# Kernel optimization log

Hardware: AMD Instinct MI355X
Metric: run time of the kernel (lower is better)

## Reference

```python
import jax, jax.numpy as jnp
import numpy as np

B, H, W, C = 8, 128, 128, 64
C3 = 3 * C            # interleaved channel count = 192
SE_R = 16             # squeeze-excite ratio


def setup_inputs() -> dict:
    key = jax.random.key(0)
    ks = jax.random.split(key, 7)
    t1 = jax.random.normal(ks[0], (B, H, W, C), dtype=jnp.float32)
    t2 = jax.random.normal(ks[1], (B, H, W, C), dtype=jnp.float32)
    t3 = jax.random.normal(ks[2], (B, H, W, C), dtype=jnp.float32)
    # SE block: two bias-free dense layers (he_normal-ish scaling)
    w_se1 = jax.random.normal(ks[3], (C3, C3 // SE_R), dtype=jnp.float32) * np.float32(np.sqrt(2.0 / C3))
    w_se2 = jax.random.normal(ks[4], (C3 // SE_R, C3), dtype=jnp.float32) * np.float32(np.sqrt(2.0 / (C3 // SE_R)))
    # Conv3D (1,1,3) stride (1,1,3) SAME on a size-1 depth dim == middle-tap
    # 1x1 conv: only kernel[...,1,:,:] multiplies real data. Keep that tap.
    w_conv = jax.random.normal(ks[5], (C3, C), dtype=jnp.float32) * np.float32(np.sqrt(1.0 / C3))
    b_conv = jnp.zeros((C,), dtype=jnp.float32)
    return {"t1": t1, "t2": t2, "t3": t3, "w_se1": w_se1, "w_se2": w_se2,
            "w_conv": w_conv, "b_conv": b_conv}


def reference(t1, t2, t3, w_se1, w_se2, w_conv, b_conv):
    b, h, w, c = t1.shape
    # Channel interleave: [t1_0, t2_0, t3_0, t1_1, t2_1, t3_1, ...]
    x = jnp.stack([t1, t2, t3], axis=-1).reshape(b, h, w, 3 * c)  # [B,H,W,3C]
    # Squeeze-excite: GAP -> dense(relu, no bias) -> dense(sigmoid, no bias) -> scale
    s = x.mean(axis=(1, 2))                       # [B,3C]
    s = jax.nn.relu(s @ w_se1)                    # [B,3C/16]
    s = jax.nn.sigmoid(s @ w_se2)                 # [B,3C]
    x = x * s[:, None, None, :]
    # Conv3D (1,1,3)/stride(1,1,3) SAME on depth-1 axis == per-pixel 3C->C matmul
    out = jax.nn.relu(jnp.einsum('bhwc,cf->bhwf', x, w_conv) + b_conv)  # [B,H,W,C]
    return out
```

## Files before the change

### kernel.cpp

```cpp
#include <hip/hip_runtime.h>
#include <hip/hip_bf16.h>

#define BQ   8
#define HW   16384
#define CIN  64
#define C3   192
#define KPB  64
#define TPB  4

typedef __attribute__((ext_vector_type(8))) short short8;
typedef __attribute__((ext_vector_type(4))) float f32x4;

__device__ __forceinline__ ushort f2bf(float f) {
    uint u = __float_as_uint(f);
    u += 0x7fffu + ((u >> 16) & 1u);
    return (ushort)(u >> 16);
}

__global__ __launch_bounds__(256) void k_reduce(const float* __restrict__ t1,
                                                const float* __restrict__ t2,
                                                const float* __restrict__ t3,
                                                float* __restrict__ partials) {
    const int bid  = blockIdx.x;
    const int b    = bid >> 6;
    const int kblk = bid & 63;
    const size_t base = (size_t)b * (size_t)(HW * CIN) + (size_t)kblk * 16384;
    const float4* s0 = (const float4*)(t1 + base);
    const float4* s1 = (const float4*)(t2 + base);
    const float4* s2 = (const float4*)(t3 + base);
    const int tid = threadIdx.x;

    float acc[3][4] = {{0.f,0.f,0.f,0.f},{0.f,0.f,0.f,0.f},{0.f,0.f,0.f,0.f}};
#pragma unroll
    for (int i = 0; i < 16; ++i) {
        const int idx = i * 256 + tid;
        float4 v0 = s0[idx];
        float4 v1 = s1[idx];
        float4 v2 = s2[idx];
        acc[0][0] += v0.x; acc[0][1] += v0.y; acc[0][2] += v0.z; acc[0][3] += v0.w;
        acc[1][0] += v1.x; acc[1][1] += v1.y; acc[1][2] += v1.z; acc[1][3] += v1.w;
        acc[2][0] += v2.x; acc[2][1] += v2.y; acc[2][2] += v2.z; acc[2][3] += v2.w;
    }
#pragma unroll
    for (int t = 0; t < 3; ++t)
#pragma unroll
        for (int j = 0; j < 4; ++j) {
            float v = acc[t][j];
            v += __shfl_xor(v, 16);
            v += __shfl_xor(v, 32);
            acc[t][j] = v;
        }

    __shared__ float red[4][C3];
    const int lane = tid & 63, wave = tid >> 6;
    if (lane < 16) {
#pragma unroll
        for (int t = 0; t < 3; ++t)
#pragma unroll
            for (int j = 0; j < 4; ++j)
                red[wave][3 * (lane * 4 + j) + t] = acc[t][j];
    }
    __syncthreads();
    if (tid < C3) {
        float v = red[0][tid] + red[1][tid] + red[2][tid] + red[3][tid];
        partials[(size_t)(b * KPB + kblk) * C3 + tid] = v;
    }
}

__global__ __launch_bounds__(256) void k_se(const float* __restrict__ partials,
                                            const float* __restrict__ w_se1,
                                            const float* __restrict__ w_se2,
                                            const float* __restrict__ w_conv,
                                            ushort* __restrict__ wbT) {
    const int b = blockIdx.x, tid = threadIdx.x;
    __shared__ float s_lds[C3];
    __shared__ float h_lds[12];
    __shared__ float sig_lds[C3];

    if (tid < C3) {
        float s = 0.f;
        const float* p = partials + (size_t)b * KPB * C3 + tid;
        for (int k = 0; k < KPB; ++k) s += p[k * C3];
        s_lds[tid] = s * (1.f / 16384.f);
    }
    __syncthreads();
    if (tid < 12) {
        float h = 0.f;
        for (int j = 0; j < C3; ++j) h += s_lds[j] * w_se1[j * 12 + tid];
        h_lds[tid] = fmaxf(h, 0.f);
    }
    __syncthreads();
    if (tid < C3) {
        float z = 0.f;
#pragma unroll
        for (int i = 0; i < 12; ++i) z += h_lds[i] * w_se2[i * C3 + tid];
        sig_lds[tid] = 1.f / (1.f + expf(-z));
    }
    __syncthreads();
    if (tid < C3) {
        const int c = tid & 63, t = tid >> 6;
        const int c3 = 3 * c + t;
        const float g = sig_lds[c3];
        ushort* dst = wbT + (size_t)b * CIN * C3;
        for (int f = 0; f < CIN; ++f)
            dst[f * C3 + tid] = f2bf(g * w_conv[c3 * CIN + f]);
    }
}

__global__ __launch_bounds__(256) void k_main(const float* __restrict__ t1,
                                              const float* __restrict__ t2,
                                              const float* __restrict__ t3,
                                              const ushort* __restrict__ wbT,
                                              const float* __restrict__ b_conv,
                                              float* __restrict__ out) {
    __shared__ ushort xs[64 * 200];
    __shared__ ushort wt[64 * 200];

    const int bid  = blockIdx.x;
    const int b    = bid >> 6;
    const int kblk = bid & 63;
    const int tid  = threadIdx.x;
    const int lane = tid & 63, wave = tid >> 6;
    const int l16  = lane & 15, lhi = lane >> 4;

    {
        const uint2* src = (const uint2*)(wbT + (size_t)b * CIN * C3);
#pragma unroll
        for (int i = 0; i < 12; ++i) {
            int ch  = i * 256 + tid;
            int row = ch / 48, col8 = ch % 48;
            *(uint2*)&wt[row * 200 + col8 * 4] = src[ch];
        }
    }

    float bias[4];
#pragma unroll
    for (int ft = 0; ft < 4; ++ft) bias[ft] = b_conv[ft * 16 + l16];

    for (int j = 0; j < TPB; ++j) {
        const int tile = kblk + j * 64;
        const size_t pbase = (size_t)b * HW + (size_t)tile * 64;
        __syncthreads();
        const float4* src0 = (const float4*)(t1 + pbase * CIN);
        const float4* src1 = (const float4*)(t2 + pbase * CIN);
        const float4* src2 = (const float4*)(t3 + pbase * CIN);
#pragma unroll
        for (int t = 0; t < 3; ++t) {
            const float4* s = (t == 0) ? src0 : (t == 1) ? src1 : src2;
#pragma unroll
            for (int i = 0; i < 4; ++i) {
                int idx = i * 256 + tid;
                float4 v = s[idx];
                int pix = idx >> 4, c = (idx & 15) * 4;
                ushort4 pk;
                pk.x = f2bf(v.x); pk.y = f2bf(v.y);
                pk.z = f2bf(v.z); pk.w = f2bf(v.w);
                *(ushort4*)&xs[pix * 200 + t * 64 + c] = pk;
            }
        }
        __syncthreads();

        f32x4 acc[4];
#pragma unroll
        for (int ft = 0; ft < 4; ++ft) acc[ft] = (f32x4){0.f, 0.f, 0.f, 0.f};
        const int arow = wave * 16 + l16;
        const int ko   = lhi * 8;
#pragma unroll
        for (int kt = 0; kt < 6; ++kt) {
            short8 a = *(const short8*)&xs[arow * 200 + kt * 32 + ko];
#pragma unroll
            for (int ft = 0; ft < 4; ++ft) {
                short8 bb = *(const short8*)&wt[(ft * 16 + l16) * 200 + kt * 32 + ko];
                acc[ft] = __builtin_amdgcn_mfma_f32_16x16x32_bf16(a, bb, acc[ft], 0, 0, 0);
            }
        }
        const size_t obase = ((size_t)b * HW + (size_t)tile * 64 + wave * 16) * CIN;
#pragma unroll
        for (int ft = 0; ft < 4; ++ft) {
#pragma unroll
            for (int r = 0; r < 4; ++r) {
                float v = acc[ft][r] + bias[ft];
                v = fmaxf(v, 0.f);
                out[obase + (size_t)(lhi * 4 + r) * CIN + ft * 16 + l16] = v;
            }
        }
    }
}

extern "C" void kernel_launch(void* const* d_in, const int* in_sizes, int n_in,
                              void* d_out, int out_size, void* d_ws, size_t ws_size,
                              hipStream_t stream) {
    (void)in_sizes; (void)n_in; (void)out_size; (void)ws_size;
    const float* t1     = (const float*)d_in[0];
    const float* t2     = (const float*)d_in[1];
    const float* t3     = (const float*)d_in[2];
    const float* w_se1  = (const float*)d_in[3];
    const float* w_se2  = (const float*)d_in[4];
    const float* w_conv = (const float*)d_in[5];
    const float* b_conv = (const float*)d_in[6];
    float* out = (float*)d_out;

    float*  partials = (float*)d_ws;
    ushort* wbT      = (ushort*)((char*)d_ws + 512 * C3 * 4);

    k_reduce<<<dim3(BQ * KPB), dim3(256), 0, stream>>>(t1, t2, t3, partials);
    k_se<<<dim3(BQ), dim3(256), 0, stream>>>(partials, w_se1, w_se2, w_conv, wbT);
    k_main<<<dim3(BQ * KPB), dim3(256), 0, stream>>>(t1, t2, t3, wbT, b_conv, out);
}
```

Before: 169.6 us.

## Fuse reduce, SE and conv into one cooperative kernel with register-held inputs

Adds a cooperative-launch kernel where each block loads its 256 pixels of all three inputs once, accumulates the channel sums, and keeps the bf16-packed data in registers. A grid-wide sync then lets every block compute the SE gates itself, build its scaled weight tile in LDS, and run the MFMA matmul from the register copy. This removes the second read of the 100MB input and the intermediate kernel launches. In exchange it holds 96 registers of data per thread, does redundant SE work in every block, and depends on all 512 blocks being co-resident, falling back to the three-kernel path otherwise.

```diff
diff --git a/kernel.cpp b/kernel.cpp
--- a/kernel.cpp
+++ b/kernel.cpp
@@ -1,12 +1,14 @@
 #include <hip/hip_runtime.h>
 #include <hip/hip_bf16.h>
+#include <hip/hip_cooperative_groups.h>
+
+namespace cg = cooperative_groups;
 
 #define BQ   8
 #define HW   16384
 #define CIN  64
 #define C3   192
 #define KPB  64
-#define TPB  4
 
 typedef __attribute__((ext_vector_type(8))) short short8;
 typedef __attribute__((ext_vector_type(4))) float f32x4;
@@ -15,6 +17,151 @@
     uint u = __float_as_uint(f);
     u += 0x7fffu + ((u >> 16) & 1u);
     return (ushort)(u >> 16);
+}
+
+__global__ __launch_bounds__(256, 2) void k_fused(
+        const float* __restrict__ t1, const float* __restrict__ t2,
+        const float* __restrict__ t3,
+        const float* __restrict__ w_se1, const float* __restrict__ w_se2,
+        const float* __restrict__ w_conv, const float* __restrict__ b_conv,
+        float* __restrict__ partials, float* __restrict__ out) {
+    __shared__ __align__(16) ushort smem[2 * 64 * 200];
+    ushort* xs = smem;
+    ushort* wt = smem + 64 * 200;
+    float* red   = (float*)smem;
+    float* smean = (float*)smem + 4 * C3;
+    float* hbuf  = (float*)smem + 5 * C3;
+    float* sigb  = (float*)smem + 5 * C3 + 12;
+
+    const int bid  = blockIdx.x;
+    const int b    = bid >> 6;
+    const int kblk = bid & 63;
+    const int tid  = threadIdx.x;
+    const int lane = tid & 63, wave = tid >> 6;
+    const int l16  = lane & 15, lhi = lane >> 4;
+
+    uint dreg[4][3][8];
+    float acc[3][4] = {{0.f,0.f,0.f,0.f},{0.f,0.f,0.f,0.f},{0.f,0.f,0.f,0.f}};
+    const size_t pixbase = (size_t)b * HW + (size_t)kblk * 256;
+#pragma unroll
+    for (int j = 0; j < 4; ++j) {
+        const size_t cb = (pixbase + (size_t)j * 64) * CIN;
+        const float4* s0 = (const float4*)(t1 + cb);
+        const float4* s1 = (const float4*)(t2 + cb);
+        const float4* s2 = (const float4*)(t3 + cb);
+#pragma unroll
+        for (int t = 0; t < 3; ++t) {
+            const float4* s = (t == 0) ? s0 : (t == 1) ? s1 : s2;
+#pragma unroll
+            for (int i = 0; i < 4; ++i) {
+                float4 v = s[i * 256 + tid];
+                acc[t][0] += v.x; acc[t][1] += v.y;
+                acc[t][2] += v.z; acc[t][3] += v.w;
+                dreg[j][t][i * 2]     = (uint)f2bf(v.x) | ((uint)f2bf(v.y) << 16);
+                dreg[j][t][i * 2 + 1] = (uint)f2bf(v.z) | ((uint)f2bf(v.w) << 16);
+            }
+        }
+    }
+#pragma unroll
+    for (int t = 0; t < 3; ++t)
+#pragma unroll
+        for (int jj = 0; jj < 4; ++jj) {
+            float v = acc[t][jj];
+            v += __shfl_xor(v, 16);
+            v += __shfl_xor(v, 32);
+            acc[t][jj] = v;
+        }
+    if (lane < 16) {
+#pragma unroll
+        for (int t = 0; t < 3; ++t)
+#pragma unroll
+            for (int jj = 0; jj < 4; ++jj)
+                red[wave * C3 + 3 * (l16 * 4 + jj) + t] = acc[t][jj];
+    }
+    __syncthreads();
+    if (tid < C3) {
+        float v = red[0 * C3 + tid] + red[1 * C3 + tid] +
+                  red[2 * C3 + tid] + red[3 * C3 + tid];
+        partials[(size_t)bid * C3 + tid] = v;
+    }
+    __threadfence();
+    cg::this_grid().sync();
+
+    if (tid < C3) {
+        const float* p = partials + (size_t)(b * KPB) * C3 + tid;
+        float s = 0.f;
+#pragma unroll 8
+        for (int k = 0; k < KPB; ++k) s += p[k * C3];
+        smean[tid] = s * (1.f / 16384.f);
+    }
+    __syncthreads();
+    if (tid < 12) {
+        float h = 0.f;
+        for (int j = 0; j < C3; ++j) h += smean[j] * w_se1[j * 12 + tid];
+        hbuf[tid] = fmaxf(h, 0.f);
+    }
+    __syncthreads();
+    if (tid < C3) {
+        float z = 0.f;
+#pragma unroll
+        for (int i = 0; i < 12; ++i) z += hbuf[i] * w_se2[i * C3 + tid];
+        sigb[tid] = 1.f / (1.f + expf(-z));
+    }
+    __syncthreads();
+    if (tid < C3) {
+        const int c = tid & 63, t = tid >> 6;
+        const int c3 = 3 * c + t;
+        const float g = sigb[c3];
+#pragma unroll
+        for (int f = 0; f < CIN; ++f)
+            wt[f * 200 + tid] = f2bf(g * w_conv[c3 * CIN + f]);
+    }
+    float bias[4];
+#pragma unroll
+    for (int ft = 0; ft < 4; ++ft) bias[ft] = b_conv[ft * 16 + l16];
+    __syncthreads();
+
+#pragma unroll
+    for (int j = 0; j < 4; ++j) {
+        if (j) __syncthreads();
+#pragma unroll
+        for (int t = 0; t < 3; ++t)
+#pragma unroll
+            for (int i = 0; i < 4; ++i) {
+                const int idx = i * 256 + tid;
+                const int pix = idx >> 4, c = (idx & 15) * 4;
+                uint2 w;
+                w.x = dreg[j][t][i * 2];
+                w.y = dreg[j][t][i * 2 + 1];
+                *(uint2*)&xs[pix * 200 + t * 64 + c] = w;
+            }
+        __syncthreads();
+
+        f32x4 a4[4];
+#pragma unroll
+        for (int ft = 0; ft < 4; ++ft) a4[ft] = (f32x4){0.f, 0.f, 0.f, 0.f};
+        const int arow = wave * 16 + l16;
+        const int ko   = lhi * 8;
+#pragma unroll
+        for (int kt = 0; kt < 6; ++kt) {
+            short8 a = *(const short8*)&xs[arow * 200 + kt * 32 + ko];
+#pragma unroll
+            for (int ft = 0; ft < 4; ++ft) {
+                short8 bb = *(const short8*)&wt[(ft * 16 + l16) * 200 + kt * 32 + ko];
+                a4[ft] = __builtin_amdgcn_mfma_f32_16x16x32_bf16(a, bb, a4[ft], 0, 0, 0);
+            }
+        }
+        const size_t obase = (pixbase + (size_t)j * 64 + wave * 16) * CIN;
+#pragma unroll
+        for (int ft = 0; ft < 4; ++ft) {
+#pragma unroll
+            for (int r = 0; r < 4; ++r) {
+                float v = a4[ft][r] + bias[ft];
+                v = fmaxf(v, 0.f);
+                out[obase + (size_t)(lhi * 4 + r) * CIN + ft * 16 + l16] = v;
+            }
+        }
+    }
 }
 
 __global__ __launch_bounds__(256) void k_reduce(const float* __restrict__ t1,
@@ -58,7 +205,7 @@
         for (int t = 0; t < 3; ++t)
 #pragma unroll
             for (int j = 0; j < 4; ++j)
-                red[wave][3 * (lane * 4 + j) + t] = acc[t][j];
+                red[wave][3 * ((lane & 15) * 4 + j) + t] = acc[t][j];
     }
     __syncthreads();
     if (tid < C3) {
@@ -137,7 +284,7 @@
 #pragma unroll
     for (int ft = 0; ft < 4; ++ft) bias[ft] = b_conv[ft * 16 + l16];
 
-    for (int j = 0; j < TPB; ++j) {
+    for (int j = 0; j < 4; ++j) {
         const int tile = kblk + j * 64;
         const size_t pbase = (size_t)b * HW + (size_t)tile * 64;
         __syncthreads();
@@ -160,9 +307,9 @@
         }
         __syncthreads();
 
-        f32x4 acc[4];
-#pragma unroll
-        for (int ft = 0; ft < 4; ++ft) acc[ft] = (f32x4){0.f, 0.f, 0.f, 0.f};
+        f32x4 a4[4];
+#pragma unroll
+        for (int ft = 0; ft < 4; ++ft) a4[ft] = (f32x4){0.f, 0.f, 0.f, 0.f};
         const int arow = wave * 16 + l16;
         const int ko   = lhi * 8;
 #pragma unroll
@@ -171,7 +318,7 @@
 #pragma unroll
             for (int ft = 0; ft < 4; ++ft) {
                 short8 bb = *(const short8*)&wt[(ft * 16 + l16) * 200 + kt * 32 + ko];
-                acc[ft] = __builtin_amdgcn_mfma_f32_16x16x32_bf16(a, bb, acc[ft], 0, 0, 0);
+                a4[ft] = __builtin_amdgcn_mfma_f32_16x16x32_bf16(a, bb, a4[ft], 0, 0, 0);
             }
         }
         const size_t obase = ((size_t)b * HW + (size_t)tile * 64 + wave * 16) * CIN;
@@ -179,7 +326,7 @@
         for (int ft = 0; ft < 4; ++ft) {
 #pragma unroll
             for (int r = 0; r < 4; ++r) {
-                float v = acc[ft][r] + bias[ft];
+                float v = a4[ft][r] + bias[ft];
                 v = fmaxf(v, 0.f);
                 out[obase + (size_t)(lhi * 4 + r) * CIN + ft * 16 + l16] = v;
             }
@@ -203,6 +350,23 @@
     float*  partials = (float*)d_ws;
     ushort* wbT      = (ushort*)((char*)d_ws + 512 * C3 * 4);
 
+    int dev = 0, numCU = 0, occ = 0;
+    hipGetDevice(&dev);
+    hipDeviceGetAttribute(&numCU, hipDeviceAttributeMultiprocessorCount, dev);
+    hipOccupancyMaxActiveBlocksPerMultiprocessor(&occ, (const void*)k_fused, 256, 0);
+
+    if (occ * numCU >= BQ * KPB) {
+        void* args[] = {
+            (void*)&t1, (void*)&t2, (void*)&t3,
+            (void*)&w_se1, (void*)&w_se2, (void*)&w_conv, (void*)&b_conv,
+            (void*)&partials, (void*)&out,
+        };
+        hipError_t e = hipLaunchCooperativeKernel((const void*)k_fused,
+                                                  dim3(BQ * KPB), dim3(256),
+                                                  args, 0, stream);
+        if (e == hipSuccess) return;
+    }
+
     k_reduce<<<dim3(BQ * KPB), dim3(256), 0, stream>>>(t1, t2, t3, partials);
     k_se<<<dim3(BQ), dim3(256), 0, stream>>>(partials, w_se1, w_se2, w_conv, wbT);
     k_main<<<dim3(BQ * KPB), dim3(256), 0, stream>>>(t1, t2, t3, wbT, b_conv, out);
```

New measurement: 173.0 us. +2.0%, slower.

## Materialize bf16 interleaved activations during reduction pass and read them in conv

Applied to the files above, without the earlier changes.

The reduction kernel now also converts inputs to bf16 and writes an interleaved 3C-channel copy to workspace. The conv kernel reads this compact copy directly from global memory instead of re-reading and converting the three fp32 inputs through shared memory. The aim is to halve the second read of activations. In exchange it adds a 48 MB workspace write and strided global A-operand loads, and it needs a larger workspace.

```diff
diff --git a/kernel.cpp b/kernel.cpp
--- a/kernel.cpp
+++ b/kernel.cpp
@@ -6,7 +6,6 @@
 #define CIN  64
 #define C3   192
 #define KPB  64
-#define TPB  4
 
 typedef __attribute__((ext_vector_type(8))) short short8;
 typedef __attribute__((ext_vector_type(4))) float f32x4;
@@ -17,53 +16,64 @@
     return (ushort)(u >> 16);
 }
 
-__global__ __launch_bounds__(256) void k_reduce(const float* __restrict__ t1,
-                                                const float* __restrict__ t2,
-                                                const float* __restrict__ t3,
-                                                float* __restrict__ partials) {
+__global__ __launch_bounds__(256) void k_prep(const float* __restrict__ t1,
+                                              const float* __restrict__ t2,
+                                              const float* __restrict__ t3,
+                                              ushort* __restrict__ xws,
+                                              float* __restrict__ partials) {
     const int bid  = blockIdx.x;
     const int b    = bid >> 6;
     const int kblk = bid & 63;
-    const size_t base = (size_t)b * (size_t)(HW * CIN) + (size_t)kblk * 16384;
-    const float4* s0 = (const float4*)(t1 + base);
-    const float4* s1 = (const float4*)(t2 + base);
-    const float4* s2 = (const float4*)(t3 + base);
-    const int tid = threadIdx.x;
+    const int tid  = threadIdx.x;
+    const int lane = tid & 63, wave = tid >> 6;
+    const int l16  = lane & 15;
 
+    const size_t pixbase = (size_t)b * HW + (size_t)kblk * 256;
     float acc[3][4] = {{0.f,0.f,0.f,0.f},{0.f,0.f,0.f,0.f},{0.f,0.f,0.f,0.f}};
+
 #pragma unroll
-    for (int i = 0; i < 16; ++i) {
-        const int idx = i * 256 + tid;
-        float4 v0 = s0[idx];
-        float4 v1 = s1[idx];
-        float4 v2 = s2[idx];
-        acc[0][0] += v0.x; acc[0][1] += v0.y; acc[0][2] += v0.z; acc[0][3] += v0.w;
-        acc[1][0] += v1.x; acc[1][1] += v1.y; acc[1][2] += v1.z; acc[1][3] += v1.w;
-        acc[2][0] += v2.x; acc[2][1] += v2.y; acc[2][2] += v2.z; acc[2][3] += v2.w;
+    for (int j = 0; j < 4; ++j) {
+        const size_t cb = (pixbase + (size_t)j * 64) * CIN;
+        ushort* xw = xws + (pixbase + (size_t)j * 64) * C3;
+#pragma unroll
+        for (int t = 0; t < 3; ++t) {
+            const float* base = (t == 0) ? t1 : (t == 1) ? t2 : t3;
+            const float4* s = (const float4*)(base + cb);
+#pragma unroll
+            for (int i = 0; i < 4; ++i) {
+                const int idx = i * 256 + tid;
+                float4 v = s[idx];
+                acc[t][0] += v.x; acc[t][1] += v.y;
+                acc[t][2] += v.z; acc[t][3] += v.w;
+                const int pix = idx >> 4, c = (idx & 15) * 4;
+                ushort4 pk;
+                pk.x = f2bf(v.x); pk.y = f2bf(v.y);
+                pk.z = f2bf(v.z); pk.w = f2bf(v.w);
+                *(ushort4*)&xw[pix * C3 + t * CIN + c] = pk;
+            }
+        }
     }
 #pragma unroll
     for (int t = 0; t < 3; ++t)
 #pragma unroll
-        for (int j = 0; j < 4; ++j) {
-            float v = acc[t][j];
+        for (int jj = 0; jj < 4; ++jj) {
+            float v = acc[t][jj];
             v += __shfl_xor(v, 16);
             v += __shfl_xor(v, 32);
-            acc[t][j] = v;
+            acc[t][jj] = v;
         }
-
     __shared__ float red[4][C3];
-    const int lane = tid & 63, wave = tid >> 6;
     if (lane < 16) {
 #pragma unroll
         for (int t = 0; t < 3; ++t)
 #pragma unroll
-            for (int j = 0; j < 4; ++j)
-                red[wave][3 * (lane * 4 + j) + t] = acc[t][j];
+            for (int jj = 0; jj < 4; ++jj)
+                red[wave][3 * (l16 * 4 + jj) + t] = acc[t][jj];
     }
     __syncthreads();
     if (tid < C3) {
         float v = red[0][tid] + red[1][tid] + red[2][tid] + red[3][tid];
-        partials[(size_t)(b * KPB + kblk) * C3 + tid] = v;
+        partials[(size_t)bid * C3 + tid] = v;
     }
 }
 
@@ -107,13 +117,10 @@
     }
 }
 
-__global__ __launch_bounds__(256) void k_main(const float* __restrict__ t1,
-                                              const float* __restrict__ t2,
-                                              const float* __restrict__ t3,
+__global__ __launch_bounds__(256) void k_conv(const ushort* __restrict__ xws,
                                               const ushort* __restrict__ wbT,
                                               const float* __restrict__ b_conv,
                                               float* __restrict__ out) {
-    __shared__ ushort xs[64 * 200];
     __shared__ ushort wt[64 * 200];
 
     const int bid  = blockIdx.x;
@@ -132,54 +139,35 @@
             *(uint2*)&wt[row * 200 + col8 * 4] = src[ch];
         }
     }
-
     float bias[4];
 #pragma unroll
     for (int ft = 0; ft < 4; ++ft) bias[ft] = b_conv[ft * 16 + l16];
+    __syncthreads();
 
-    for (int j = 0; j < TPB; ++j) {
-        const int tile = kblk + j * 64;
-        const size_t pbase = (size_t)b * HW + (size_t)tile * 64;
-        __syncthreads();
-        const float4* src0 = (const float4*)(t1 + pbase * CIN);
-        const float4* src1 = (const float4*)(t2 + pbase * CIN);
-        const float4* src2 = (const float4*)(t3 + pbase * CIN);
+    const size_t pixbase = (size_t)b * HW + (size_t)kblk * 256;
 #pragma unroll
-        for (int t = 0; t < 3; ++t) {
-            const float4* s = (t == 0) ? src0 : (t == 1) ? src1 : src2;
+    for (int j = 0; j < 4; ++j) {
+        const size_t prow = pixbase + (size_t)j * 64 + wave * 16 + l16;
+        const ushort* arow = xws + prow * C3;
+
+        f32x4 a4[4];
 #pragma unroll
-            for (int i = 0; i < 4; ++i) {
-                int idx = i * 256 + tid;
-                float4 v = s[idx];
-                int pix = idx >> 4, c = (idx & 15) * 4;
-                ushort4 pk;
-                pk.x = f2bf(v.x); pk.y = f2bf(v.y);
-                pk.z = f2bf(v.z); pk.w = f2bf(v.w);
-                *(ushort4*)&xs[pix * 200 + t * 64 + c] = pk;
+        for (int ft = 0; ft < 4; ++ft) a4[ft] = (f32x4){0.f, 0.f, 0.f, 0.f};
+#pragma unroll
+        for (int kt = 0; kt < 6; ++kt) {
+            short8 a = *(const short8*)&arow[kt * 32 + lhi * 8];
+#pragma unroll
+            for (int ft = 0; ft < 4; ++ft) {
+                short8 bb = *(const short8*)&wt[(ft * 16 + l16) * 200 + kt * 32 + lhi * 8];
+                a4[ft] = __builtin_amdgcn_mfma_f32_16x16x32_bf16(a, bb, a4[ft], 0, 0, 0);
             }
         }
-        __syncthreads();
-
-        f32x4 acc[4];
-#pragma unroll
-        for (int ft = 0; ft < 4; ++ft) acc[ft] = (f32x4){0.f, 0.f, 0.f, 0.f};
-        const int arow = wave * 16 + l16;
-        const int ko   = lhi * 8;
-#pragma unroll
-        for (int kt = 0; kt < 6; ++kt) {
-            short8 a = *(const short8*)&xs[arow * 200 + kt * 32 + ko];
-#pragma unroll
-            for (int ft = 0; ft < 4; ++ft) {
-                short8 bb = *(const short8*)&wt[(ft * 16 + l16) * 200 + kt * 32 + ko];
-                acc[ft] = __builtin_amdgcn_mfma_f32_16x16x32_bf16(a, bb, acc[ft], 0, 0, 0);
-            }
-        }
-        const size_t obase = ((size_t)b * HW + (size_t)tile * 64 + wave * 16) * CIN;
+        const size_t obase = (pixbase + (size_t)j * 64 + wave * 16) * CIN;
 #pragma unroll
         for (int ft = 0; ft < 4; ++ft) {
 #pragma unroll
             for (int r = 0; r < 4; ++r) {
-                float v = acc[ft][r] + bias[ft];
+                float v = a4[ft][r] + bias[ft];
                 v = fmaxf(v, 0.f);
                 out[obase + (size_t)(lhi * 4 + r) * CIN + ft * 16 + l16] = v;
             }
@@ -202,8 +190,9 @@
 
     float*  partials = (float*)d_ws;
     ushort* wbT      = (ushort*)((char*)d_ws + 512 * C3 * 4);
+    ushort* xws      = (ushort*)((char*)d_ws + 1024 * 1024);
 
-    k_reduce<<<dim3(BQ * KPB), dim3(256), 0, stream>>>(t1, t2, t3, partials);
-    k_se<<<dim3(BQ), dim3(256), 0, stream>>>(partials, w_se1, w_se2, w_conv, wbT);
-    k_main<<<dim3(BQ * KPB), dim3(256), 0, stream>>>(t1, t2, t3, wbT, b_conv, out);
+    k_prep<<<dim3(BQ * KPB), dim3(256), 0, stream>>>(t1, t2, t3, xws, partials);
+    k_se  <<<dim3(BQ),       dim3(256), 0, stream>>>(partials, w_se1, w_se2, w_conv, wbT);
+    k_conv<<<dim3(BQ * KPB), dim3(256), 0, stream>>>(xws, wbT, b_conv, out);
 }
```

After: 174.6 us. 3.0% more time.
